# Performance work log

Hardware: AMD Instinct MI355X
Metric: run time of the kernel (lower is better)

The kernel has to match this reference:

```python
import jax, jax.numpy as jnp
import numpy as np

BS, Z_DIM, HID, Z_IN, N_STEP, OUT_DIM = 4096, 512, 1024, 128, 32, 3


def setup_inputs() -> dict:
    key = jax.random.key(0)
    ks = jax.random.split(key, 12)
    s = 0.02
    return {
        "z": jax.random.normal(ks[0], (BS, Z_DIM), jnp.float32),
        "inference": 1,
        "tfr": 0,
        "W_zh": jax.random.normal(ks[1], (HID, Z_DIM), jnp.float32) * s,
        "b_zh": jnp.zeros((HID,), jnp.float32),
        "W_zi": jax.random.normal(ks[2], (Z_IN, Z_DIM), jnp.float32) * s,
        "b_zi": jnp.zeros((Z_IN,), jnp.float32),
        "W_ih": jax.random.normal(ks[3], (3 * HID, OUT_DIM + Z_IN), jnp.float32) * s,
        "b_ih": jnp.zeros((3 * HID,), jnp.float32),
        "W_hh": jax.random.normal(ks[4], (3 * HID, HID), jnp.float32) * s,
        "b_hh": jnp.zeros((3 * HID,), jnp.float32),
        "W_out": jax.random.normal(ks[5], (OUT_DIM, HID), jnp.float32) * s,
        "b_out": jnp.zeros((OUT_DIM,), jnp.float32),
        "init_input": jax.random.uniform(ks[6], (OUT_DIM,), jnp.float32),
    }


def reference(z, inference, tfr, W_zh, b_zh, W_zi, b_zi, W_ih, b_ih, W_hh, b_hh,
              W_out, b_out, init_input):
    bs = z.shape[0]
    h0 = z @ W_zh.T + b_zh                      # [B, H]   (z2dec_hid)
    z_in = z @ W_zi.T + b_zi                    # [B, Z_IN] (z2dec_in)
    token0 = jnp.broadcast_to(init_input, (bs, OUT_DIM))

    def step(carry, _):
        h, token = carry
        x = jnp.concatenate([token, z_in], axis=-1)     # [B, OUT_DIM+Z_IN]
        gi = x @ W_ih.T + b_ih                          # [B, 3H]
        gh = h @ W_hh.T + b_hh                          # [B, 3H]
        i_r, i_u, i_n = jnp.split(gi, 3, axis=-1)       # pytorch gate order r,z,n
        h_r, h_u, h_n = jnp.split(gh, 3, axis=-1)
        r = jax.nn.sigmoid(i_r + h_r)
        u = jax.nn.sigmoid(i_u + h_u)
        n = jnp.tanh(i_n + r * h_n)
        h_new = (1.0 - u) * n + u * h
        o = h_new @ W_out.T + b_out                     # [B, 3]
        bass = jax.nn.sigmoid(o[:, 0])
        rhy_int = o[:, 1]
        rhy = jax.nn.sigmoid(o[:, 2])
        out_feat = jnp.stack([bass, rhy_int, rhy], axis=-1)          # [B, 3]
        next_token = jnp.stack(
            [bass, rhy_int, (rhy > 0.5).astype(z.dtype)], axis=-1)  # [B, 3]
        return (h_new, next_token), out_feat

    _, outs = jax.lax.scan(step, (h0, token0), None, length=N_STEP)  # [T, B, 3]
    recon = jnp.transpose(outs, (1, 0, 2))                           # [B, T, 3]
    return recon
```

## Files before the change

kernel.cpp:

```cpp
#include <hip/hip_runtime.h>
#include <hip/hip_bf16.h>
#include <math.h>

#define BS   4096
#define ZD   512
#define HIDN 1024
#define ZINN 128
#define NST  32
#define NP   3072

typedef unsigned short u16;
typedef __bf16 bf16x8 __attribute__((ext_vector_type(8)));
typedef _Float16 f16x8 __attribute__((ext_vector_type(8)));
typedef float f32x4 __attribute__((ext_vector_type(4)));
typedef float f32x16 __attribute__((ext_vector_type(16)));

static __device__ __forceinline__ u16 bf_bits(float v) {
  __bf16 b = (__bf16)v;
  return __builtin_bit_cast(unsigned short, b);
}
static __device__ __forceinline__ float bf_val(float v) {
  return (float)(__bf16)v;
}
static __device__ __forceinline__ u16 h16_bits(float v) {
  _Float16 h = (_Float16)v;
  return __builtin_bit_cast(unsigned short, h);
}

static __device__ __forceinline__ void ld_lds16(const u16* g, u16* l) {
  __builtin_amdgcn_global_load_lds(
      (const __attribute__((address_space(1))) void*)g,
      (__attribute__((address_space(3))) void*)l, 16, 0, 0);
}

static __device__ __forceinline__ int r_orig(int w) {
  const int g = w / 96;
  const int rem = w - g * 96;
  const int j = rem >> 5, m = rem & 31;
  return j * 1024 + g * 32 + m;
}

static __device__ __forceinline__ size_t pk_off(int row, int col) {
  return ((size_t)(row >> 5) * 64 + (col >> 4)) * 512 +
         (((col >> 3) & 1) * 32 + (row & 31)) * 8 + (col & 7);
}


__global__ void k_split(const float* __restrict__ s, u16* __restrict__ hi,
                        u16* __restrict__ lo, int n) {
  int i = blockIdx.x * 256 + threadIdx.x;
  if (i >= n) return;
  float v = s[i];
  float h = bf_val(v);
  hi[i] = bf_bits(v);
  lo[i] = bf_bits(v - h);
}

__global__ void k_pack_whh(const float* __restrict__ W_hh, u16* __restrict__ Bpk) {
  int i = blockIdx.x * 256 + threadIdx.x;
  if (i >= NP * HIDN) return;
  const int w = i >> 10, k = i & 1023;
  const float v = W_hh[(size_t)r_orig(w) * HIDN + k];
  Bpk[pk_off(w, k)] = h16_bits(v);
}

__global__ void k_prep_wih(const float* __restrict__ W_ih, const float* __restrict__ b_ih,
                           const float* __restrict__ b_hh,
                           u16* __restrict__ whi, u16* __restrict__ wlo,
                           float* __restrict__ wtok, float* __restrict__ cb0) {
  int i = blockIdx.x * 256 + threadIdx.x;
  if (i < NP * 128) {
    const int w = i >> 7, c = i & 127;
    const int r = r_orig(w);
    const float v = W_ih[r * 131 + 3 + c];
    const float h = bf_val(v);
    whi[i] = bf_bits(v);
    wlo[i] = bf_bits(v - h);
  }
  if (i < NP * 3) {
    const int w = i / 3, s = i - w * 3;
    wtok[i] = W_ih[r_orig(w) * 131 + s];
  }
  if (i < NP) {
    const int r = r_orig(i);
    cb0[i] = b_ih[r] + (r < 2048 ? b_hh[r] : 0.0f);
  }
}

__global__ void k_token_init(const float* __restrict__ init_input, float* __restrict__ token) {
  int i = blockIdx.x * 256 + threadIdx.x;
  if (i < BS * 4) token[i] = ((i & 3) < 3) ? init_input[i & 3] : 0.0f;
}

template <int OUTMODE>
__global__ __launch_bounds__(256) void k_gemm(
    const u16* __restrict__ Ahi, const u16* __restrict__ Alo,
    const u16* __restrict__ Bhi, const u16* __restrict__ Blo,
    const float* __restrict__ bias,
    float* __restrict__ C, u16* __restrict__ Chi, u16* __restrict__ Clo,
    u16* __restrict__ Apk, int N, int K) {
  __shared__ __align__(16) u16 sAhi[128 * 64];
  __shared__ __align__(16) u16 sAlo[128 * 64];
  __shared__ __align__(16) u16 sBhi[128 * 64];
  __shared__ __align__(16) u16 sBlo[128 * 64];

  const int t = threadIdx.x;
  const int row0 = blockIdx.y * 128, col0 = blockIdx.x * 128;
  const int wave = t >> 6, lane = t & 63;
  const int w64 = wave * 64;
  const int wm = (wave & 1) * 64, wn = (wave >> 1) * 64;
  const int lm = lane & 15, lq = lane >> 4;
  const int pb = lm & 7;

  f32x4 acc[4][4] = {};

  int sm[4], skc[4], sub[4];
#pragma unroll
  for (int i = 0; i < 4; ++i) {
    const int u = i * 256 + t;
    sm[i] = u >> 3;
    skc[i] = (u & 7) ^ (sm[i] & 7);
    sub[i] = (i * 256 + w64) * 8;
  }

  const int nk = K >> 6;
  for (int kt = 0; kt < nk; ++kt) {
    const int k0 = kt << 6;
    __syncthreads();
#pragma unroll
    for (int i = 0; i < 4; ++i) {
      const size_t ga = (size_t)(row0 + sm[i]) * K + k0 + skc[i] * 8;
      const size_t gb = (size_t)(col0 + sm[i]) * K + k0 + skc[i] * 8;
      ld_lds16(Ahi + ga, &sAhi[sub[i]]);
      ld_lds16(Alo + ga, &sAlo[sub[i]]);
      ld_lds16(Bhi + gb, &sBhi[sub[i]]);
      ld_lds16(Blo + gb, &sBlo[sub[i]]);
    }
    __syncthreads();
#pragma unroll
    for (int kk = 0; kk < 2; ++kk) {
      const int pos = ((kk * 4 + lq) ^ pb) * 8;
      bf16x8 ah[4], al[4], bh[4], bl[4];
#pragma unroll
      for (int i = 0; i < 4; ++i) {
        const int ma = (wm + i * 16 + lm) * 64;
        const int mb = (wn + i * 16 + lm) * 64;
        ah[i] = *(const bf16x8*)&sAhi[ma + pos];
        al[i] = *(const bf16x8*)&sAlo[ma + pos];
        bh[i] = *(const bf16x8*)&sBhi[mb + pos];
        bl[i] = *(const bf16x8*)&sBlo[mb + pos];
      }
#pragma unroll
      for (int i = 0; i < 4; ++i)
#pragma unroll
        for (int j = 0; j < 4; ++j) {
          acc[i][j] = __builtin_amdgcn_mfma_f32_16x16x32_bf16(ah[i], bh[j], acc[i][j], 0, 0, 0);
          acc[i][j] = __builtin_amdgcn_mfma_f32_16x16x32_bf16(al[i], bh[j], acc[i][j], 0, 0, 0);
          acc[i][j] = __builtin_amdgcn_mfma_f32_16x16x32_bf16(ah[i], bl[j], acc[i][j], 0, 0, 0);
        }
    }
  }

#pragma unroll
  for (int i = 0; i < 4; ++i) {
    const int grow = row0 + wm + i * 16 + lq * 4;
#pragma unroll
    for (int j = 0; j < 4; ++j) {
      const int gcol = col0 + wn + j * 16 + lm;
      const float bs = bias ? bias[gcol] : 0.0f;
#pragma unroll
      for (int d = 0; d < 4; ++d) {
        const float v = acc[i][j][d] + bs;
        const size_t idx = (size_t)(grow + d) * N + gcol;
        C[idx] = v;
        if (OUTMODE == 1) {
          const float h = bf_val(v);
          Chi[idx] = bf_bits(v);
          Clo[idx] = bf_bits(v - h);
        }
        if (OUTMODE == 2) {
          Apk[pk_off(grow + d, gcol)] = h16_bits(v);
        }
      }
    }
  }
}


#define SZA8 (128 * 64)
#define SZB8 (192 * 64)
#define MF8(a, b, c) c = __builtin_amdgcn_mfma_f32_32x32x16_f16(a, b, c, 0, 0, 0)

__global__ __launch_bounds__(512, 4) void k_fused8(
    const u16* __restrict__ Apk,
    const u16* __restrict__ Bpk,
    const float* __restrict__ C0,
    const float* __restrict__ token,
    const float* __restrict__ wtok,
    const float* __restrict__ b_hh,
    const float* __restrict__ h_in, float* __restrict__ h_out,
    u16* __restrict__ Apk_out) {
  __shared__ __align__(16) u16 sA[2 * SZA8];
  __shared__ __align__(16) u16 sB[2 * SZB8];

  const int t = threadIdx.x;
  const int wave = t >> 6, lane = t & 63;
  const int row0 = blockIdx.y * 128;
  const int colW0 = blockIdx.x * 192;
  const int wm = (wave >> 1) * 32;
  const int wn = (wave & 1) * 96;
  const int lr = lane & 31, lh = lane >> 5;

  f32x16 acc0 = {}, acc1 = {}, acc2 = {};

  const u16* asrc = Apk + ((size_t)((row0 >> 5) + (wave >> 1)) * 64 + (wave & 1) * 2) * 512 + lane * 8;
  const int aw = (wave >> 1) * 2048 + (wave & 1) * 1024;
  const int id0 = wave * 3, id1 = id0 + 1, id2 = id0 + 2;
  const u16* bsrc0 = Bpk + ((size_t)((colW0 >> 5) + (id0 >> 2)) * 64 + (id0 & 3)) * 512 + lane * 8;
  const u16* bsrc1 = Bpk + ((size_t)((colW0 >> 5) + (id1 >> 2)) * 64 + (id1 & 3)) * 512 + lane * 8;
  const u16* bsrc2 = Bpk + ((size_t)((colW0 >> 5) + (id2 >> 2)) * 64 + (id2 & 3)) * 512 + lane * 8;
  const int bw0 = id0 * 512, bw1 = id1 * 512, bw2 = id2 * 512;

#define STAGE(kt_, ab, bb)                                            \
  ld_lds16(asrc + (size_t)(kt_) * 2048,       &sA[(ab) + aw]);        \
  ld_lds16(asrc + (size_t)(kt_) * 2048 + 512, &sA[(ab) + aw + 512]);  \
  ld_lds16(bsrc0 + (size_t)(kt_) * 2048, &sB[(bb) + bw0]);            \
  ld_lds16(bsrc1 + (size_t)(kt_) * 2048, &sB[(bb) + bw1]);            \
  ld_lds16(bsrc2 + (size_t)(kt_) * 2048, &sB[(bb) + bw2]);

  const int agA = (wave >> 1) * 2048;
  const int bgB = (wave & 1) * 6144;
  const int l8 = lane * 8;

  STAGE(0, 0, 0);
  __syncthreads();

#pragma unroll 1
  for (int kt = 0; kt < 16; ++kt) {
    const int ab = (kt & 1) ? SZA8 : 0, bb = (kt & 1) ? SZB8 : 0;
    const int an = (kt & 1) ? 0 : SZA8, bn = (kt & 1) ? 0 : SZB8;
    if (kt < 15) { STAGE(kt + 1, an, bn); }
#pragma unroll
    for (int kk = 0; kk < 4; ++kk) {
      const f16x8 a = *(const f16x8*)&sA[ab + agA + kk * 512 + l8];
      const int kb = bb + bgB + kk * 512 + l8;
      const f16x8 b0 = *(const f16x8*)&sB[kb];
      const f16x8 b1 = *(const f16x8*)&sB[kb + 2048];
      const f16x8 b2 = *(const f16x8*)&sB[kb + 4096];
      MF8(a, b0, acc0); MF8(a, b1, acc1); MF8(a, b2, acc2);
    }
    __syncthreads();
  }
#undef STAGE

  const int w0 = colW0 + wn + lr;
  const int c = ((colW0 + wn) / 96) * 32 + lr;
  float wt[3][3];
#pragma unroll
  for (int j = 0; j < 3; ++j) {
    wt[j][0] = wtok[(w0 + j * 32) * 3 + 0];
    wt[j][1] = wtok[(w0 + j * 32) * 3 + 1];
    wt[j][2] = wtok[(w0 + j * 32) * 3 + 2];
  }
  const float bn = b_hh[2048 + c];
  const int cq = c >> 4, ckh = (c >> 3) & 1, ce = c & 7;
#pragma unroll
  for (int d = 0; d < 16; ++d) {
    const int row = row0 + wm + 4 * lh + (d & 3) + 8 * (d >> 2);
    const float4 tk = *(const float4*)&token[row * 4];
    const size_t cb = (size_t)row * NP;
    const float pr = C0[cb + w0]      + acc0[d] + tk.x * wt[0][0] + tk.y * wt[0][1] + tk.z * wt[0][2];
    const float pu = C0[cb + w0 + 32] + acc1[d] + tk.x * wt[1][0] + tk.y * wt[1][1] + tk.z * wt[1][2];
    const float pn = C0[cb + w0 + 64] + tk.x * wt[2][0] + tk.y * wt[2][1] + tk.z * wt[2][2];
    const float hn = acc2[d] + bn;
    const float r = 1.0f / (1.0f + expf(-pr));
    const float u = 1.0f / (1.0f + expf(-pu));
    const float n = tanhf(pn + r * hn);
    const size_t hidx = (size_t)row * HIDN + c;
    const float hv = (1.0f - u) * n + u * h_in[hidx];
    h_out[hidx] = hv;
    const size_t poff = ((size_t)(row >> 5) * 64 + cq) * 512 + (ckh * 32 + (row & 31)) * 8 + ce;
    Apk_out[poff] = h16_bits(hv);
  }
}
#undef MF8

__global__ __launch_bounds__(256) void k_out(
    const float* __restrict__ h, const float* __restrict__ W_out,
    const float* __restrict__ b_out,
    float* __restrict__ out, float* __restrict__ token, int step) {
  const int wave = threadIdx.x >> 6, lane = threadIdx.x & 63;
  const int row = blockIdx.x * 4 + wave;
  const float4* hp = (const float4*)(h + (size_t)row * 1024);
  const float4* w0p = (const float4*)(W_out);
  const float4* w1p = (const float4*)(W_out + 1024);
  const float4* w2p = (const float4*)(W_out + 2048);
  float s0 = 0.f, s1 = 0.f, s2 = 0.f;
#pragma unroll
  for (int c = 0; c < 4; ++c) {
    const int k = lane + 64 * c;
    const float4 hv = hp[k];
    const float4 a = w0p[k], bq = w1p[k], cq = w2p[k];
    s0 += hv.x * a.x + hv.y * a.y + hv.z * a.z + hv.w * a.w;
    s1 += hv.x * bq.x + hv.y * bq.y + hv.z * bq.z + hv.w * bq.w;
    s2 += hv.x * cq.x + hv.y * cq.y + hv.z * cq.z + hv.w * cq.w;
  }
#pragma unroll
  for (int off = 32; off > 0; off >>= 1) {
    s0 += __shfl_xor(s0, off, 64);
    s1 += __shfl_xor(s1, off, 64);
    s2 += __shfl_xor(s2, off, 64);
  }
  if (lane == 0) {
    const float o0 = s0 + b_out[0];
    const float o1 = s1 + b_out[1];
    const float o2 = s2 + b_out[2];
    const float bass = 1.0f / (1.0f + expf(-o0));
    const float rhy = 1.0f / (1.0f + expf(-o2));
    const size_t ob = ((size_t)row * NST + step) * 3;
    out[ob + 0] = bass;
    out[ob + 1] = o1;
    out[ob + 2] = rhy;
    token[row * 4 + 0] = bass;
    token[row * 4 + 1] = o1;
    token[row * 4 + 2] = (rhy > 0.5f) ? 1.0f : 0.0f;
  }
}

extern "C" void kernel_launch(void* const* d_in, const int* in_sizes, int n_in,
                              void* d_out, int out_size, void* d_ws, size_t ws_size,
                              hipStream_t stream) {
  const float* z = (const float*)d_in[0];
  const float* W_zh = (const float*)d_in[3];
  const float* b_zh = (const float*)d_in[4];
  const float* W_zi = (const float*)d_in[5];
  const float* b_zi = (const float*)d_in[6];
  const float* W_ih = (const float*)d_in[7];
  const float* b_ih = (const float*)d_in[8];
  const float* W_hh = (const float*)d_in[9];
  const float* b_hh = (const float*)d_in[10];
  const float* W_out = (const float*)d_in[11];
  const float* b_out = (const float*)d_in[12];
  const float* init_input = (const float*)d_in[13];
  float* out = (float*)d_out;

  char* p = (char*)d_ws;
  auto alloc = [&](size_t bytes) {
    char* q = p;
    p += (bytes + 255) & ~(size_t)255;
    return q;
  };
  float* h[2];
  u16* Apk[2];
  for (int s = 0; s < 2; ++s) {
    h[s] = (float*)alloc((size_t)BS * HIDN * 4);
    Apk[s] = (u16*)alloc((size_t)BS * 1024 * 2);
  }
  float* C0 = (float*)alloc((size_t)BS * NP * 4);
  u16* z_hi = (u16*)alloc((size_t)BS * ZD * 2);
  u16* z_lo = (u16*)alloc((size_t)BS * ZD * 2);
  float* zin = (float*)alloc((size_t)BS * ZINN * 4);
  u16* zin_hi = (u16*)alloc((size_t)BS * ZINN * 2);
  u16* zin_lo = (u16*)alloc((size_t)BS * ZINN * 2);
  u16* Wzh_hi = (u16*)alloc((size_t)HIDN * ZD * 2);
  u16* Wzh_lo = (u16*)alloc((size_t)HIDN * ZD * 2);
  u16* Wzi_hi = (u16*)alloc((size_t)ZINN * ZD * 2);
  u16* Wzi_lo = (u16*)alloc((size_t)ZINN * ZD * 2);
  u16* Wihz_hi = (u16*)alloc((size_t)NP * ZINN * 2);
  u16* Wihz_lo = (u16*)alloc((size_t)NP * ZINN * 2);
  u16* Bpk = (u16*)alloc((size_t)NP * 1024 * 2);
  float* wtok = (float*)alloc((size_t)NP * 3 * 4);
  float* cb0 = (float*)alloc((size_t)NP * 4);
  float* token = (float*)alloc((size_t)BS * 4 * 4);

  k_pack_whh<<<dim3((NP * HIDN + 255) / 256), 256, 0, stream>>>(W_hh, Bpk);
  k_split<<<dim3((HIDN * ZD + 255) / 256), 256, 0, stream>>>(W_zh, Wzh_hi, Wzh_lo, HIDN * ZD);
  k_split<<<dim3((ZINN * ZD + 255) / 256), 256, 0, stream>>>(W_zi, Wzi_hi, Wzi_lo, ZINN * ZD);
  k_split<<<dim3((BS * ZD + 255) / 256), 256, 0, stream>>>(z, z_hi, z_lo, BS * ZD);
  k_prep_wih<<<dim3((NP * 128 + 255) / 256), 256, 0, stream>>>(W_ih, b_ih, b_hh, Wihz_hi, Wihz_lo, wtok, cb0);
  k_token_init<<<dim3((BS * 4 + 255) / 256), 256, 0, stream>>>(init_input, token);

  k_gemm<2><<<dim3(HIDN / 128, BS / 128), 256, 0, stream>>>(
      z_hi, z_lo, Wzh_hi, Wzh_lo, b_zh, h[0], nullptr, nullptr, Apk[0], HIDN, ZD);
  k_gemm<1><<<dim3(ZINN / 128, BS / 128), 256, 0, stream>>>(
      z_hi, z_lo, Wzi_hi, Wzi_lo, b_zi, zin, zin_hi, zin_lo, nullptr, ZINN, ZD);
  k_gemm<0><<<dim3(NP / 128, BS / 128), 256, 0, stream>>>(
      zin_hi, zin_lo, Wihz_hi, Wihz_lo, cb0, C0, nullptr, nullptr, nullptr, NP, ZINN);

  for (int t = 0; t < NST; ++t) {
    const int cur = t & 1, nxt = (t + 1) & 1;
    k_fused8<<<dim3(NP / 192, BS / 128), 512, 0, stream>>>(
        Apk[cur], Bpk, C0, token, wtok, b_hh, h[cur], h[nxt], Apk[nxt]);
    k_out<<<dim3(BS / 4), 256, 0, stream>>>(h[nxt], W_out, b_out, out, token, t);
  }
  (void)in_sizes; (void)n_in; (void)out_size; (void)ws_size;
}
```

Measured before the change: 1.743 ms.

## Fuse z_in input projection and output projection into recurrent GRU step kernel

Drops the precomputed fp32 C0 tensor (BS x 3072, re-read every step). The per-step kernel now recomputes the z_in @ W_ih input gates with two extra fp16 MFMA k-tiles fed from packed Zpk/Wpk buffers. The W_out projection is also folded into the GRU epilogue through wave shuffles and atomicAdd into a double-buffered accumulator. A small finalize kernel then applies the biases and sigmoids, writes outputs and tokens, and clears the accumulator. This trades a large per-step memory read for a little extra MFMA work, atomics, and fp16 rounding of z_in and W_ih instead of the previous hi/lo split.

```diff
diff --git a/kernel.cpp b/kernel.cpp
--- a/kernel.cpp
+++ b/kernel.cpp
@@ -42,6 +42,10 @@
 
 static __device__ __forceinline__ size_t pk_off(int row, int col) {
   return ((size_t)(row >> 5) * 64 + (col >> 4)) * 512 +
+         (((col >> 3) & 1) * 32 + (row & 31)) * 8 + (col & 7);
+}
+static __device__ __forceinline__ size_t pkz_off(int row, int col) {
+  return ((size_t)(row >> 5) * 8 + (col >> 4)) * 512 +
          (((col >> 3) & 1) * 32 + (row & 31)) * 8 + (col & 7);
 }
 
@@ -66,16 +70,13 @@
 
 __global__ void k_prep_wih(const float* __restrict__ W_ih, const float* __restrict__ b_ih,
                            const float* __restrict__ b_hh,
-                           u16* __restrict__ whi, u16* __restrict__ wlo,
+                           u16* __restrict__ Wpk,
                            float* __restrict__ wtok, float* __restrict__ cb0) {
   int i = blockIdx.x * 256 + threadIdx.x;
   if (i < NP * 128) {
     const int w = i >> 7, c = i & 127;
-    const int r = r_orig(w);
-    const float v = W_ih[r * 131 + 3 + c];
-    const float h = bf_val(v);
-    whi[i] = bf_bits(v);
-    wlo[i] = bf_bits(v - h);
+    const float v = W_ih[r_orig(w) * 131 + 3 + c];
+    Wpk[pkz_off(w, c)] = h16_bits(v);
   }
   if (i < NP * 3) {
     const int w = i / 3, s = i - w * 3;
@@ -87,9 +88,11 @@
   }
 }
 
-__global__ void k_token_init(const float* __restrict__ init_input, float* __restrict__ token) {
+__global__ void k_token_init(const float* __restrict__ init_input, float* __restrict__ token,
+                             float* __restrict__ oacc) {
   int i = blockIdx.x * 256 + threadIdx.x;
   if (i < BS * 4) token[i] = ((i & 3) < 3) ? init_input[i & 3] : 0.0f;
+  if (i < 2 * BS * 3) oacc[i] = 0.0f;
 }
 
 template <int OUTMODE>
@@ -97,8 +100,7 @@
     const u16* __restrict__ Ahi, const u16* __restrict__ Alo,
     const u16* __restrict__ Bhi, const u16* __restrict__ Blo,
     const float* __restrict__ bias,
-    float* __restrict__ C, u16* __restrict__ Chi, u16* __restrict__ Clo,
-    u16* __restrict__ Apk, int N, int K) {
+    float* __restrict__ C, u16* __restrict__ Apk, int N, int K) {
   __shared__ __align__(16) u16 sAhi[128 * 64];
   __shared__ __align__(16) u16 sAlo[128 * 64];
   __shared__ __align__(16) u16 sBhi[128 * 64];
@@ -171,15 +173,12 @@
 #pragma unroll
       for (int d = 0; d < 4; ++d) {
         const float v = acc[i][j][d] + bs;
-        const size_t idx = (size_t)(grow + d) * N + gcol;
-        C[idx] = v;
-        if (OUTMODE == 1) {
-          const float h = bf_val(v);
-          Chi[idx] = bf_bits(v);
-          Clo[idx] = bf_bits(v - h);
+        if (OUTMODE == 2) {
+          C[(size_t)(grow + d) * N + gcol] = v;
+          Apk[pk_off(grow + d, gcol)] = h16_bits(v);
         }
-        if (OUTMODE == 2) {
-          Apk[pk_off(grow + d, gcol)] = h16_bits(v);
+        if (OUTMODE == 3) {
+          Apk[pkz_off(grow + d, gcol)] = h16_bits(v);
         }
       }
     }
@@ -191,15 +190,19 @@
 #define SZB8 (192 * 64)
 #define MF8(a, b, c) c = __builtin_amdgcn_mfma_f32_32x32x16_f16(a, b, c, 0, 0, 0)
 
-__global__ __launch_bounds__(512, 4) void k_fused8(
+__global__ __launch_bounds__(512, 4) void k_fused9(
     const u16* __restrict__ Apk,
     const u16* __restrict__ Bpk,
-    const float* __restrict__ C0,
+    const u16* __restrict__ Zpk,
+    const u16* __restrict__ Wpk,
     const float* __restrict__ token,
     const float* __restrict__ wtok,
+    const float* __restrict__ cb0,
     const float* __restrict__ b_hh,
+    const float* __restrict__ W_out,
     const float* __restrict__ h_in, float* __restrict__ h_out,
-    u16* __restrict__ Apk_out) {
+    u16* __restrict__ Apk_out,
+    float* __restrict__ oacc) {
   __shared__ __align__(16) u16 sA[2 * SZA8];
   __shared__ __align__(16) u16 sB[2 * SZB8];
 
@@ -211,7 +214,7 @@
   const int wn = (wave & 1) * 96;
   const int lr = lane & 31, lh = lane >> 5;
 
-  f32x16 acc0 = {}, acc1 = {}, acc2 = {};
+  f32x16 acc0 = {}, acc1 = {}, acc2 = {}, acc3 = {};
 
   const u16* asrc = Apk + ((size_t)((row0 >> 5) + (wave >> 1)) * 64 + (wave & 1) * 2) * 512 + lane * 8;
   const int aw = (wave >> 1) * 2048 + (wave & 1) * 1024;
@@ -220,6 +223,10 @@
   const u16* bsrc1 = Bpk + ((size_t)((colW0 >> 5) + (id1 >> 2)) * 64 + (id1 & 3)) * 512 + lane * 8;
   const u16* bsrc2 = Bpk + ((size_t)((colW0 >> 5) + (id2 >> 2)) * 64 + (id2 & 3)) * 512 + lane * 8;
   const int bw0 = id0 * 512, bw1 = id1 * 512, bw2 = id2 * 512;
+  const u16* azb = Zpk + ((size_t)((row0 >> 5) + (wave >> 1)) * 8 + (wave & 1) * 2) * 512 + lane * 8;
+  const u16* bzb0 = Wpk + ((size_t)((colW0 >> 5) + (id0 >> 2)) * 8 + (id0 & 3)) * 512 + lane * 8;
+  const u16* bzb1 = Wpk + ((size_t)((colW0 >> 5) + (id1 >> 2)) * 8 + (id1 & 3)) * 512 + lane * 8;
+  const u16* bzb2 = Wpk + ((size_t)((colW0 >> 5) + (id2 >> 2)) * 8 + (id2 & 3)) * 512 + lane * 8;
 
 #define STAGE(kt_, ab, bb)                                            \
   ld_lds16(asrc + (size_t)(kt_) * 2048,       &sA[(ab) + aw]);        \
@@ -228,6 +235,13 @@
   ld_lds16(bsrc1 + (size_t)(kt_) * 2048, &sB[(bb) + bw1]);            \
   ld_lds16(bsrc2 + (size_t)(kt_) * 2048, &sB[(bb) + bw2]);
 
+#define STAGE_Z(zt_, ab, bb)                                          \
+  ld_lds16(azb + (zt_) * 2048,       &sA[(ab) + aw]);                 \
+  ld_lds16(azb + (zt_) * 2048 + 512, &sA[(ab) + aw + 512]);           \
+  ld_lds16(bzb0 + (zt_) * 2048, &sB[(bb) + bw0]);                     \
+  ld_lds16(bzb1 + (zt_) * 2048, &sB[(bb) + bw1]);                     \
+  ld_lds16(bzb2 + (zt_) * 2048, &sB[(bb) + bw2]);
+
   const int agA = (wave >> 1) * 2048;
   const int bgB = (wave & 1) * 6144;
   const int l8 = lane * 8;
@@ -240,6 +254,7 @@
     const int ab = (kt & 1) ? SZA8 : 0, bb = (kt & 1) ? SZB8 : 0;
     const int an = (kt & 1) ? 0 : SZA8, bn = (kt & 1) ? 0 : SZB8;
     if (kt < 15) { STAGE(kt + 1, an, bn); }
+    else         { STAGE_Z(0, an, bn); }
 #pragma unroll
     for (int kk = 0; kk < 4; ++kk) {
       const f16x8 a = *(const f16x8*)&sA[ab + agA + kk * 512 + l8];
@@ -251,7 +266,28 @@
     }
     __syncthreads();
   }
+  STAGE_Z(1, SZA8, SZB8);
+#pragma unroll
+  for (int kk = 0; kk < 4; ++kk) {
+    const f16x8 a = *(const f16x8*)&sA[agA + kk * 512 + l8];
+    const int kb = bgB + kk * 512 + l8;
+    const f16x8 b0 = *(const f16x8*)&sB[kb];
+    const f16x8 b1 = *(const f16x8*)&sB[kb + 2048];
+    const f16x8 b2 = *(const f16x8*)&sB[kb + 4096];
+    MF8(a, b0, acc0); MF8(a, b1, acc1); MF8(a, b2, acc3);
+  }
+  __syncthreads();
+#pragma unroll
+  for (int kk = 0; kk < 4; ++kk) {
+    const f16x8 a = *(const f16x8*)&sA[SZA8 + agA + kk * 512 + l8];
+    const int kb = SZB8 + bgB + kk * 512 + l8;
+    const f16x8 b0 = *(const f16x8*)&sB[kb];
+    const f16x8 b1 = *(const f16x8*)&sB[kb + 2048];
+    const f16x8 b2 = *(const f16x8*)&sB[kb + 4096];
+    MF8(a, b0, acc0); MF8(a, b1, acc1); MF8(a, b2, acc3);
+  }
 #undef STAGE
+#undef STAGE_Z
 
   const int w0 = colW0 + wn + lr;
   const int c = ((colW0 + wn) / 96) * 32 + lr;
@@ -262,69 +298,69 @@
     wt[j][1] = wtok[(w0 + j * 32) * 3 + 1];
     wt[j][2] = wtok[(w0 + j * 32) * 3 + 2];
   }
-  const float bn = b_hh[2048 + c];
+  const float cbr = cb0[w0], cbu = cb0[w0 + 32], cbn = cb0[w0 + 64];
+  const float bnn = b_hh[2048 + c];
+  const float wo0 = W_out[c], wo1 = W_out[1024 + c], wo2 = W_out[2048 + c];
   const int cq = c >> 4, ckh = (c >> 3) & 1, ce = c & 7;
 #pragma unroll
   for (int d = 0; d < 16; ++d) {
     const int row = row0 + wm + 4 * lh + (d & 3) + 8 * (d >> 2);
     const float4 tk = *(const float4*)&token[row * 4];
-    const size_t cb = (size_t)row * NP;
-    const float pr = C0[cb + w0]      + acc0[d] + tk.x * wt[0][0] + tk.y * wt[0][1] + tk.z * wt[0][2];
-    const float pu = C0[cb + w0 + 32] + acc1[d] + tk.x * wt[1][0] + tk.y * wt[1][1] + tk.z * wt[1][2];
-    const float pn = C0[cb + w0 + 64] + tk.x * wt[2][0] + tk.y * wt[2][1] + tk.z * wt[2][2];
-    const float hn = acc2[d] + bn;
+    const float pr = cbr + acc0[d] + tk.x * wt[0][0] + tk.y * wt[0][1] + tk.z * wt[0][2];
+    const float pu = cbu + acc1[d] + tk.x * wt[1][0] + tk.y * wt[1][1] + tk.z * wt[1][2];
+    const float pin = cbn + acc3[d] + tk.x * wt[2][0] + tk.y * wt[2][1] + tk.z * wt[2][2];
+    const float hn = acc2[d] + bnn;
     const float r = 1.0f / (1.0f + expf(-pr));
     const float u = 1.0f / (1.0f + expf(-pu));
-    const float n = tanhf(pn + r * hn);
+    const float n = tanhf(pin + r * hn);
     const size_t hidx = (size_t)row * HIDN + c;
     const float hv = (1.0f - u) * n + u * h_in[hidx];
     h_out[hidx] = hv;
     const size_t poff = ((size_t)(row >> 5) * 64 + cq) * 512 + (ckh * 32 + (row & 31)) * 8 + ce;
     Apk_out[poff] = h16_bits(hv);
+    acc0[d] = hv * wo0;
+    acc1[d] = hv * wo1;
+    acc3[d] = hv * wo2;
+  }
+#pragma unroll
+  for (int d = 0; d < 16; ++d) {
+    float s0 = acc0[d], s1 = acc1[d], s2 = acc3[d];
+#pragma unroll
+    for (int off = 1; off <= 16; off <<= 1) {
+      s0 += __shfl_xor(s0, off, 64);
+      s1 += __shfl_xor(s1, off, 64);
+      s2 += __shfl_xor(s2, off, 64);
+    }
+    if (lr == 0) {
+      const int row = row0 + wm + 4 * lh + (d & 3) + 8 * (d >> 2);
+      atomicAdd(&oacc[row * 3 + 0], s0);
+      atomicAdd(&oacc[row * 3 + 1], s1);
+      atomicAdd(&oacc[row * 3 + 2], s2);
+    }
   }
 }
 #undef MF8
 
-__global__ __launch_bounds__(256) void k_out(
-    const float* __restrict__ h, const float* __restrict__ W_out,
-    const float* __restrict__ b_out,
+__global__ __launch_bounds__(256) void k_finalize(
+    float* __restrict__ oacc, const float* __restrict__ b_out,
     float* __restrict__ out, float* __restrict__ token, int step) {
-  const int wave = threadIdx.x >> 6, lane = threadIdx.x & 63;
-  const int row = blockIdx.x * 4 + wave;
-  const float4* hp = (const float4*)(h + (size_t)row * 1024);
-  const float4* w0p = (const float4*)(W_out);
-  const float4* w1p = (const float4*)(W_out + 1024);
-  const float4* w2p = (const float4*)(W_out + 2048);
-  float s0 = 0.f, s1 = 0.f, s2 = 0.f;
-#pragma unroll
-  for (int c = 0; c < 4; ++c) {
-    const int k = lane + 64 * c;
-    const float4 hv = hp[k];
-    const float4 a = w0p[k], bq = w1p[k], cq = w2p[k];
-    s0 += hv.x * a.x + hv.y * a.y + hv.z * a.z + hv.w * a.w;
-    s1 += hv.x * bq.x + hv.y * bq.y + hv.z * bq.z + hv.w * bq.w;
-    s2 += hv.x * cq.x + hv.y * cq.y + hv.z * cq.z + hv.w * cq.w;
-  }
-#pragma unroll
-  for (int off = 32; off > 0; off >>= 1) {
-    s0 += __shfl_xor(s0, off, 64);
-    s1 += __shfl_xor(s1, off, 64);
-    s2 += __shfl_xor(s2, off, 64);
-  }
-  if (lane == 0) {
-    const float o0 = s0 + b_out[0];
-    const float o1 = s1 + b_out[1];
-    const float o2 = s2 + b_out[2];
-    const float bass = 1.0f / (1.0f + expf(-o0));
-    const float rhy = 1.0f / (1.0f + expf(-o2));
-    const size_t ob = ((size_t)row * NST + step) * 3;
-    out[ob + 0] = bass;
-    out[ob + 1] = o1;
-    out[ob + 2] = rhy;
-    token[row * 4 + 0] = bass;
-    token[row * 4 + 1] = o1;
-    token[row * 4 + 2] = (rhy > 0.5f) ? 1.0f : 0.0f;
-  }
+  const int row = blockIdx.x * 256 + threadIdx.x;
+  if (row >= BS) return;
+  const float o0 = oacc[row * 3 + 0] + b_out[0];
+  const float o1 = oacc[row * 3 + 1] + b_out[1];
+  const float o2 = oacc[row * 3 + 2] + b_out[2];
+  oacc[row * 3 + 0] = 0.0f;
+  oacc[row * 3 + 1] = 0.0f;
+  oacc[row * 3 + 2] = 0.0f;
+  const float bass = 1.0f / (1.0f + expf(-o0));
+  const float rhy = 1.0f / (1.0f + expf(-o2));
+  const size_t ob = ((size_t)row * NST + step) * 3;
+  out[ob + 0] = bass;
+  out[ob + 1] = o1;
+  out[ob + 2] = rhy;
+  token[row * 4 + 0] = bass;
+  token[row * 4 + 1] = o1;
+  token[row * 4 + 2] = (rhy > 0.5f) ? 1.0f : 0.0f;
 }
 
 extern "C" void kernel_launch(void* const* d_in, const int* in_sizes, int n_in,
@@ -356,42 +392,39 @@
     h[s] = (float*)alloc((size_t)BS * HIDN * 4);
     Apk[s] = (u16*)alloc((size_t)BS * 1024 * 2);
   }
-  float* C0 = (float*)alloc((size_t)BS * NP * 4);
+  u16* Bpk = (u16*)alloc((size_t)NP * 1024 * 2);
+  u16* Zpk = (u16*)alloc((size_t)BS * 128 * 2);
+  u16* Wpk = (u16*)alloc((size_t)NP * 128 * 2);
   u16* z_hi = (u16*)alloc((size_t)BS * ZD * 2);
   u16* z_lo = (u16*)alloc((size_t)BS * ZD * 2);
-  float* zin = (float*)alloc((size_t)BS * ZINN * 4);
-  u16* zin_hi = (u16*)alloc((size_t)BS * ZINN * 2);
-  u16* zin_lo = (u16*)alloc((size_t)BS * ZINN * 2);
   u16* Wzh_hi = (u16*)alloc((size_t)HIDN * ZD * 2);
   u16* Wzh_lo = (u16*)alloc((size_t)HIDN * ZD * 2);
   u16* Wzi_hi = (u16*)alloc((size_t)ZINN * ZD * 2);
   u16* Wzi_lo = (u16*)alloc((size_t)ZINN * ZD * 2);
-  u16* Wihz_hi = (u16*)alloc((size_t)NP * ZINN * 2);
-  u16* Wihz_lo = (u16*)alloc((size_t)NP * ZINN * 2);
-  u16* Bpk = (u16*)alloc((size_t)NP * 1024 * 2);
   float* wtok = (float*)alloc((size_t)NP * 3 * 4);
   float* cb0 = (float*)alloc((size_t)NP * 4);
   float* token = (float*)alloc((size_t)BS * 4 * 4);
+  float* oacc = (float*)alloc((size_t)2 * BS * 3 * 4);
 
   k_pack_whh<<<dim3((NP * HIDN + 255) / 256), 256, 0, stream>>>(W_hh, Bpk);
   k_split<<<dim3((HIDN * ZD + 255) / 256), 256, 0, stream>>>(W_zh, Wzh_hi, Wzh_lo, HIDN * ZD);
   k_split<<<dim3((ZINN * ZD + 255) / 256), 256, 0, stream>>>(W_zi, Wzi_hi, Wzi_lo, ZINN * ZD);
   k_split<<<dim3((BS * ZD + 255) / 256), 256, 0, stream>>>(z, z_hi, z_lo, BS * ZD);
-  k_prep_wih<<<dim3((NP * 128 + 255) / 256), 256, 0, stream>>>(W_ih, b_ih, b_hh, Wihz_hi, Wihz_lo, wtok, cb0);
-  k_token_init<<<dim3((BS * 4 + 255) / 256), 256, 0, stream>>>(init_input, token);
+  k_prep_wih<<<dim3((NP * 128 + 255) / 256), 256, 0, stream>>>(W_ih, b_ih, b_hh, Wpk, wtok, cb0);
+  k_token_init<<<dim3((2 * BS * 3 + 255) / 256), 256, 0, stream>>>(init_input, token, oacc);
 
   k_gemm<2><<<dim3(HIDN / 128, BS / 128), 256, 0, stream>>>(
-      z_hi, z_lo, Wzh_hi, Wzh_lo, b_zh, h[0], nullptr, nullptr, Apk[0], HIDN, ZD);
-  k_gemm<1><<<dim3(ZINN / 128, BS / 128), 256, 0, stream>>>(
-      z_hi, z_lo, Wzi_hi, Wzi_lo, b_zi, zin, zin_hi, zin_lo, nullptr, ZINN, ZD);
-  k_gemm<0><<<dim3(NP / 128, BS / 128), 256, 0, stream>>>(
-      zin_hi, zin_lo, Wihz_hi, Wihz_lo, cb0, C0, nullptr, nullptr, nullptr, NP, ZINN);
+      z_hi, z_lo, Wzh_hi, Wzh_lo, b_zh, h[0], Apk[0], HIDN, ZD);
+  k_gemm<3><<<dim3(ZINN / 128, BS / 128), 256, 0, stream>>>(
+      z_hi, z_lo, Wzi_hi, Wzi_lo, b_zi, nullptr, Zpk, ZINN, ZD);
 
   for (int t = 0; t < NST; ++t) {
     const int cur = t & 1, nxt = (t + 1) & 1;
-    k_fused8<<<dim3(NP / 192, BS / 128), 512, 0, stream>>>(
-        Apk[cur], Bpk, C0, token, wtok, b_hh, h[cur], h[nxt], Apk[nxt]);
-    k_out<<<dim3(BS / 4), 256, 0, stream>>>(h[nxt], W_out, b_out, out, token, t);
+    float* oa = oacc + (size_t)(t & 1) * BS * 3;
+    k_fused9<<<dim3(NP / 192, BS / 128), 512, 0, stream>>>(
+        Apk[cur], Bpk, Zpk, Wpk, token, wtok, cb0, b_hh, W_out,
+        h[cur], h[nxt], Apk[nxt], oa);
+    k_finalize<<<dim3(BS / 256), 256, 0, stream>>>(oa, b_out, out, token, t);
   }
   (void)in_sizes; (void)n_in; (void)out_size; (void)ws_size;
 }
```

New measurement: 2.514 ms. 44.2% more time.
